# Kernel tuning notes

Hardware: AMD Instinct MI355X
Metric: run time of the kernel (lower is better)

## Reference

```python
import jax, jax.numpy as jnp
import numpy as np

N_NODES = 30000
N_EDGES = 480000
NEG_SLOPE = 0.2  # PyG GATConv default negative_slope


def setup_inputs() -> dict:
    key = jax.random.key(0)
    ks = jax.random.split(key, 10)

    def glorot(k, shape, fan):
        return jax.random.normal(k, shape, jnp.float32) * (1.0 / np.sqrt(fan))

    x = jax.random.normal(ks[0], (N_NODES, 1024), jnp.float32)
    edge_index = jax.random.randint(ks[1], (2, N_EDGES), 0, N_NODES)
    # layer 1: in=1024 -> heads=8, C=64, concat -> 512
    W1 = glorot(ks[2], (1024, 512), 1024)
    a1_src = glorot(ks[3], (8, 64), 64)
    a1_dst = glorot(ks[4], (8, 64), 64)
    b1 = jnp.zeros((512,), jnp.float32)
    # layer 2: in=512 -> heads=1, C=256, no concat
    W2 = glorot(ks[5], (512, 256), 512)
    a2_src = glorot(ks[6], (1, 256), 256)
    a2_dst = glorot(ks[7], (1, 256), 256)
    b2 = jnp.zeros((256,), jnp.float32)
    return {"x": x, "edge_index": edge_index, "W1": W1, "a1_src": a1_src,
            "a1_dst": a1_dst, "b1": b1, "W2": W2, "a2_src": a2_src,
            "a2_dst": a2_dst, "b2": b2}


def gat_conv(x, src, dst, W, a_src, a_dst, bias, heads, channels, concat):
    """PyG-style GATConv (self-loops already included in src/dst)."""
    n = x.shape[0]
    h = (x @ W).reshape(n, heads, channels)          # [N, H, C]
    al_s = jnp.einsum('nhc,hc->nh', h, a_src)        # per-node src logits
    al_d = jnp.einsum('nhc,hc->nh', h, a_dst)        # per-node dst logits
    e = jax.nn.leaky_relu(al_s[src] + al_d[dst], NEG_SLOPE)   # [E, H]
    # segment softmax over edges grouped by destination node
    m = jax.ops.segment_max(e, dst, num_segments=n)
    p = jnp.exp(e - m[dst])
    s = jax.ops.segment_sum(p, dst, num_segments=n)
    alpha = p / s[dst]                               # [E, H]
    out = jax.ops.segment_sum(alpha[:, :, None] * h[src], dst, num_segments=n)
    out = out.reshape(n, heads * channels) if concat else out.mean(axis=1)
    return out + bias


def reference(x, edge_index, W1, a1_src, a1_dst, b1, W2, a2_src, a2_dst, b2):
    n = x.shape[0]
    loops = jnp.arange(n, dtype=edge_index.dtype)
    src = jnp.concatenate([edge_index[0], loops])    # add self-loops (PyG default)
    dst = jnp.concatenate([edge_index[1], loops])
    # eval mode: dropout is identity
    h = jax.nn.elu(gat_conv(x, src, dst, W1, a1_src, a1_dst, b1, 8, 64, True))
    out = gat_conv(h, src, dst, W2, a2_src, a2_dst, b2, 1, 256, False)
    return out
```

## Files before the change

kernel.cpp:

```cpp
#include <hip/hip_runtime.h>
#include <hip/hip_bf16.h>

typedef unsigned int uint;
typedef unsigned short ushort;
typedef __attribute__((ext_vector_type(8))) short short8;
typedef __attribute__((ext_vector_type(4))) short short4v;
typedef __attribute__((ext_vector_type(4))) float f32x4;

#define LEAKY 0.2f

__device__ __forceinline__ ushort f2bf(float f) {
  __hip_bfloat16 h = __float2bfloat16(f);
  return __builtin_bit_cast(ushort, h);
}
__device__ __forceinline__ float bf2f(ushort u) {
  uint v = ((uint)u) << 16;
  return __builtin_bit_cast(float, v);
}
__device__ __forceinline__ void gload_lds16(const void* g, void* l) {
  __builtin_amdgcn_global_load_lds(
      (const __attribute__((address_space(1))) void*)g,
      (__attribute__((address_space(3))) void*)l, 16, 0, 0);
}

__global__ void convw(const float* __restrict__ W, ushort* __restrict__ Wt,
                      int K, int N) {
  int idx = blockIdx.x * 256 + threadIdx.x;
  if (idx >= K * N) return;
  int nrow = idx / K;
  int k = idx - nrow * K;
  Wt[idx] = f2bf(W[(size_t)k * N + nrow]);
}

__global__ void zero2(int* a, int* b, int n) {
  int i = blockIdx.x * 256 + threadIdx.x;
  if (i < n) { a[i] = 0; b[i] = 0; }
}

__global__ void hist(const int* __restrict__ dst, int E, int n, int* cnt) {
  int e = blockIdx.x * 256 + threadIdx.x;
  if (e >= E + n) return;
  int d = (e < E) ? dst[e] : (e - E);
  atomicAdd(&cnt[d], 1);
}

__global__ __launch_bounds__(1024) void scan_fast(const int* __restrict__ cnt,
                                                  int* __restrict__ rp, int n) {
  __shared__ int wsum[16];
  __shared__ int woff[16];
  const int t = threadIdx.x;
  const int per = (n + 1023) / 1024;
  const int base = t * per;
  int local[32];
  int s = 0;
#pragma unroll
  for (int i = 0; i < 32; i++) {
    if (i >= per) break;
    int idx = base + i;
    int v = (idx < n) ? cnt[idx] : 0;
    local[i] = s;
    s += v;
  }
  const int lane = t & 63, wave = t >> 6;
  int incl = s;
#pragma unroll
  for (int off = 1; off < 64; off <<= 1) {
    int v = __shfl_up(incl, off);
    if (lane >= off) incl += v;
  }
  if (lane == 63) wsum[wave] = incl;
  __syncthreads();
  if (wave == 0 && lane < 16) {
    int v = wsum[lane];
    int wi = v;
#pragma unroll
    for (int off = 1; off < 16; off <<= 1) {
      int u = __shfl_up(wi, off);
      if (lane >= off) wi += u;
    }
    woff[lane] = wi - v;
  }
  __syncthreads();
  const int gexcl = woff[wave] + (incl - s);
#pragma unroll
  for (int i = 0; i < 32; i++) {
    if (i >= per) break;
    int idx = base + i;
    if (idx < n) rp[idx] = gexcl + local[i];
  }
  if (t == 1023) rp[n] = woff[15] + incl;
}

__global__ void scatter(const int* __restrict__ src, const int* __restrict__ dst,
                        int E, int n, const int* __restrict__ rp,
                        int* fill, int* __restrict__ csr) {
  int e = blockIdx.x * 256 + threadIdx.x;
  if (e >= E + n) return;
  int s, d;
  if (e < E) { s = src[e]; d = dst[e]; } else { s = d = e - E; }
  int pos = rp[d] + atomicAdd(&fill[d], 1);
  csr[pos] = s;
}

template <int ABYTES>
__global__ __launch_bounds__(512) void gemm_wide(
    const void* __restrict__ Av, const ushort* __restrict__ Bt,
    ushort* __restrict__ C, int M, int K, int N) {
  constexpr int BM = 128, BN = 256, BK = 32;
  constexpr int SPRA = (BK * ABYTES) / 16;
  constexpr int A_ITER = (BM * SPRA) / 512;
  __shared__ __align__(16) char As[2][BM * BK * ABYTES];
  __shared__ __align__(16) char Bs[2][BN * BK * 2];
  const int tid = threadIdx.x;
  const int wave = tid >> 6, lane = tid & 63;
  const int g = lane >> 4, r16 = lane & 15;

  const int nwg = (int)gridDim.x;
  const int q = nwg >> 3, r = nwg & 7;
  const int xcd = (int)blockIdx.x & 7, pos = (int)blockIdx.x >> 3;
  const int wgid = (xcd < r ? xcd * (q + 1) : r * (q + 1) + (xcd - r) * q) + pos;

  const int nby = N / BN;
  const int bx = wgid / nby;
  const int by = wgid - bx * nby;
  const int bm = bx * BM, bn = by * BN;
  const int wm = (wave >> 2) * 64, wn = (wave & 3) * 64;

  f32x4 acc[4][4] = {};
  const char* A = (const char*)Av;

  auto stage = [&](int k0, int b) {
#pragma unroll
    for (int i = 0; i < A_ITER; i++) {
      int slot = i * 512 + tid;
      int row = slot / SPRA;
      int cp = slot % SPRA;
      int key = (ABYTES == 4) ? (row & 7) : ((row >> 1) & 3);
      int cl = cp ^ key;
      int arow = bm + row;
      arow = arow < M ? arow : M - 1;
      const char* gp = A + ((size_t)arow * K + k0) * ABYTES + cl * 16;
      char* lp = &As[b][0] + (i * 512 + wave * 64) * 16;
      gload_lds16(gp, lp);
    }
#pragma unroll
    for (int i = 0; i < 2; i++) {
      int slot = i * 512 + tid;
      int row = slot >> 2;
      int cp = slot & 3;
      int cl = cp ^ ((row >> 1) & 3);
      const char* gp = (const char*)(Bt + (size_t)(bn + row) * K + k0 + cl * 8);
      char* lp = &Bs[b][0] + (i * 512 + wave * 64) * 16;
      gload_lds16(gp, lp);
    }
  };

  const int nt = K / BK;
  stage(0, 0);
  int cur = 0;
  for (int t = 0; t < nt; ++t) {
    if (t + 1 < nt) {
      stage((t + 1) * BK, cur ^ 1);
      if constexpr (ABYTES == 4)
        asm volatile("s_waitcnt vmcnt(4)" ::: "memory");
      else
        asm volatile("s_waitcnt vmcnt(3)" ::: "memory");
    } else {
      asm volatile("s_waitcnt vmcnt(0)" ::: "memory");
    }
    __builtin_amdgcn_sched_barrier(0);
    __builtin_amdgcn_s_barrier();

    short8 af[4], bfr[4];
#pragma unroll
    for (int mi = 0; mi < 4; mi++) {
      int row = wm + mi * 16 + r16;
      if constexpr (ABYTES == 4) {
        int key = row & 7;
        f32x4 lo = *(const f32x4*)(&As[cur][0] + (row * 8 + ((2 * g) ^ key)) * 16);
        f32x4 hi = *(const f32x4*)(&As[cur][0] + (row * 8 + ((2 * g + 1) ^ key)) * 16);
        short8 s;
#pragma unroll
        for (int qq = 0; qq < 4; qq++) {
          s[qq] = (short)f2bf(lo[qq]);
          s[qq + 4] = (short)f2bf(hi[qq]);
        }
        af[mi] = s;
      } else {
        int key = (row >> 1) & 3;
        af[mi] = *(const short8*)(&As[cur][0] + (row * 4 + (g ^ key)) * 16);
      }
    }
#pragma unroll
    for (int ni = 0; ni < 4; ni++) {
      int row = wn + ni * 16 + r16;
      int key = (row >> 1) & 3;
      bfr[ni] = *(const short8*)(&Bs[cur][0] + (row * 4 + (g ^ key)) * 16);
    }
#pragma unroll
    for (int mi = 0; mi < 4; mi++)
#pragma unroll
      for (int ni = 0; ni < 4; ni++)
        acc[mi][ni] = __builtin_amdgcn_mfma_f32_16x16x32_bf16(
            af[mi], bfr[ni], acc[mi][ni], 0, 0, 0);
    __builtin_amdgcn_s_barrier();
    cur ^= 1;
  }

#pragma unroll
  for (int mi = 0; mi < 4; mi++) {
#pragma unroll
    for (int j = 0; j < 4; j++) {
      int row = bm + wm + mi * 16 + g * 4 + j;
      if (row < M) {
#pragma unroll
        for (int ni = 0; ni < 4; ni++) {
          int col = bn + wn + ni * 16 + r16;
          C[(size_t)row * N + col] = f2bf(acc[mi][ni][j]);
        }
      }
    }
  }
}

__global__ void logits1(const ushort* __restrict__ h1, const float* __restrict__ a_s,
                        const float* __restrict__ a_d, float* __restrict__ al_s,
                        float* __restrict__ al_d, int n) {
  int node = blockIdx.x * 4 + (threadIdx.x >> 6);
  if (node >= n) return;
  int lane = threadIdx.x & 63;
  int c0 = lane * 8;
  short8 hv = *(const short8*)&h1[(size_t)node * 512 + c0];
  float ps = 0.f, pd = 0.f;
#pragma unroll
  for (int j = 0; j < 8; j++) {
    float f = bf2f((ushort)hv[j]);
    ps += f * a_s[c0 + j];
    pd += f * a_d[c0 + j];
  }
#pragma unroll
  for (int m = 1; m < 8; m <<= 1) {
    ps += __shfl_xor(ps, m);
    pd += __shfl_xor(pd, m);
  }
  if ((lane & 7) == 0) {
    al_s[node * 8 + (lane >> 3)] = ps;
    al_d[node * 8 + (lane >> 3)] = pd;
  }
}

__global__ void logits2(const ushort* __restrict__ h2, const float* __restrict__ a_s,
                        const float* __restrict__ a_d, float* __restrict__ al_s,
                        float* __restrict__ al_d, int n) {
  int node = blockIdx.x * 4 + (threadIdx.x >> 6);
  if (node >= n) return;
  int lane = threadIdx.x & 63;
  int c0 = lane * 4;
  short4v hv = *(const short4v*)&h2[(size_t)node * 256 + c0];
  float ps = 0.f, pd = 0.f;
#pragma unroll
  for (int j = 0; j < 4; j++) {
    float f = bf2f((ushort)hv[j]);
    ps += f * a_s[c0 + j];
    pd += f * a_d[c0 + j];
  }
#pragma unroll
  for (int m = 1; m < 64; m <<= 1) {
    ps += __shfl_xor(ps, m);
    pd += __shfl_xor(pd, m);
  }
  if (lane == 0) {
    al_s[node] = ps;
    al_d[node] = pd;
  }
}

__global__ void agg1(const int* __restrict__ rp, const int* __restrict__ csr,
                     const ushort* __restrict__ h1, const float* __restrict__ al_s,
                     const float* __restrict__ al_d, const float* __restrict__ b1,
                     ushort* __restrict__ h2in, int n) {
  int node = blockIdx.x * 4 + (threadIdx.x >> 6);
  if (node >= n) return;
  int lane = threadIdx.x & 63;
  int head = lane >> 3, c0 = lane * 8;
  float ad = al_d[node * 8 + head];
  int beg = rp[node], end = rp[node + 1];
  float sum = 0.f;
  float acc[8] = {};
  int j = beg;
  for (; j + 4 <= end; j += 4) {
    int s0 = csr[j], s1 = csr[j + 1], s2 = csr[j + 2], s3 = csr[j + 3];
    float e0 = al_s[s0 * 8 + head] + ad;
    float e1 = al_s[s1 * 8 + head] + ad;
    float e2 = al_s[s2 * 8 + head] + ad;
    float e3 = al_s[s3 * 8 + head] + ad;
    short8 v0 = *(const short8*)&h1[(size_t)s0 * 512 + c0];
    short8 v1 = *(const short8*)&h1[(size_t)s1 * 512 + c0];
    short8 v2 = *(const short8*)&h1[(size_t)s2 * 512 + c0];
    short8 v3 = *(const short8*)&h1[(size_t)s3 * 512 + c0];
    e0 = e0 > 0.f ? e0 : LEAKY * e0;
    e1 = e1 > 0.f ? e1 : LEAKY * e1;
    e2 = e2 > 0.f ? e2 : LEAKY * e2;
    e3 = e3 > 0.f ? e3 : LEAKY * e3;
    float p0 = __expf(e0), p1 = __expf(e1), p2 = __expf(e2), p3 = __expf(e3);
    sum += (p0 + p1) + (p2 + p3);
#pragma unroll
    for (int qq = 0; qq < 8; qq++)
      acc[qq] += p0 * bf2f((ushort)v0[qq]) + p1 * bf2f((ushort)v1[qq]) +
                 p2 * bf2f((ushort)v2[qq]) + p3 * bf2f((ushort)v3[qq]);
  }
  for (; j < end; j++) {
    int s = csr[j];
    float e = al_s[s * 8 + head] + ad;
    e = e > 0.f ? e : LEAKY * e;
    float p = __expf(e);
    sum += p;
    short8 hv = *(const short8*)&h1[(size_t)s * 512 + c0];
#pragma unroll
    for (int qq = 0; qq < 8; qq++) acc[qq] += p * bf2f((ushort)hv[qq]);
  }
  float inv = 1.0f / sum;
  short8 o;
#pragma unroll
  for (int qq = 0; qq < 8; qq++) {
    float rr = acc[qq] * inv + b1[c0 + qq];
    rr = rr > 0.f ? rr : (__expf(rr) - 1.0f);
    o[qq] = (short)f2bf(rr);
  }
  *(short8*)&h2in[(size_t)node * 512 + c0] = o;
}

__global__ void agg2(const int* __restrict__ rp, const int* __restrict__ csr,
                     const ushort* __restrict__ h2, const float* __restrict__ al_s,
                     const float* __restrict__ al_d, const float* __restrict__ b2,
                     float* __restrict__ out, int n) {
  int node = blockIdx.x * 4 + (threadIdx.x >> 6);
  if (node >= n) return;
  int lane = threadIdx.x & 63;
  int c0 = lane * 4;
  float ad = al_d[node];
  int beg = rp[node], end = rp[node + 1];
  float sum = 0.f;
  float a0 = 0.f, a1 = 0.f, a2 = 0.f, a3 = 0.f;
  int j = beg;
  for (; j + 4 <= end; j += 4) {
    int s0 = csr[j], s1 = csr[j + 1], s2 = csr[j + 2], s3 = csr[j + 3];
    float e0 = al_s[s0] + ad;
    float e1 = al_s[s1] + ad;
    float e2 = al_s[s2] + ad;
    float e3 = al_s[s3] + ad;
    short4v v0 = *(const short4v*)&h2[(size_t)s0 * 256 + c0];
    short4v v1 = *(const short4v*)&h2[(size_t)s1 * 256 + c0];
    short4v v2 = *(const short4v*)&h2[(size_t)s2 * 256 + c0];
    short4v v3 = *(const short4v*)&h2[(size_t)s3 * 256 + c0];
    e0 = e0 > 0.f ? e0 : LEAKY * e0;
    e1 = e1 > 0.f ? e1 : LEAKY * e1;
    e2 = e2 > 0.f ? e2 : LEAKY * e2;
    e3 = e3 > 0.f ? e3 : LEAKY * e3;
    float p0 = __expf(e0), p1 = __expf(e1), p2 = __expf(e2), p3 = __expf(e3);
    sum += (p0 + p1) + (p2 + p3);
    a0 += p0 * bf2f((ushort)v0[0]) + p1 * bf2f((ushort)v1[0]) +
          p2 * bf2f((ushort)v2[0]) + p3 * bf2f((ushort)v3[0]);
    a1 += p0 * bf2f((ushort)v0[1]) + p1 * bf2f((ushort)v1[1]) +
          p2 * bf2f((ushort)v2[1]) + p3 * bf2f((ushort)v3[1]);
    a2 += p0 * bf2f((ushort)v0[2]) + p1 * bf2f((ushort)v1[2]) +
          p2 * bf2f((ushort)v2[2]) + p3 * bf2f((ushort)v3[2]);
    a3 += p0 * bf2f((ushort)v0[3]) + p1 * bf2f((ushort)v1[3]) +
          p2 * bf2f((ushort)v2[3]) + p3 * bf2f((ushort)v3[3]);
  }
  for (; j < end; j++) {
    int s = csr[j];
    float e = al_s[s] + ad;
    e = e > 0.f ? e : LEAKY * e;
    float p = __expf(e);
    sum += p;
    short4v hv = *(const short4v*)&h2[(size_t)s * 256 + c0];
    a0 += p * bf2f((ushort)hv[0]);
    a1 += p * bf2f((ushort)hv[1]);
    a2 += p * bf2f((ushort)hv[2]);
    a3 += p * bf2f((ushort)hv[3]);
  }
  float inv = 1.0f / sum;
  f32x4 o;
  o[0] = a0 * inv + b2[c0 + 0];
  o[1] = a1 * inv + b2[c0 + 1];
  o[2] = a2 * inv + b2[c0 + 2];
  o[3] = a3 * inv + b2[c0 + 3];
  *(f32x4*)&out[(size_t)node * 256 + c0] = o;
}

extern "C" void kernel_launch(void* const* d_in, const int* in_sizes, int n_in,
                              void* d_out, int out_size, void* d_ws, size_t ws_size,
                              hipStream_t stream) {
  const float* x = (const float*)d_in[0];
  const int* ei = (const int*)d_in[1];
  const float* W1 = (const float*)d_in[2];
  const float* a1s = (const float*)d_in[3];
  const float* a1d = (const float*)d_in[4];
  const float* b1 = (const float*)d_in[5];
  const float* W2 = (const float*)d_in[6];
  const float* a2s = (const float*)d_in[7];
  const float* a2d = (const float*)d_in[8];
  const float* b2 = (const float*)d_in[9];
  float* out = (float*)d_out;

  const int n = in_sizes[0] / 1024;
  const int E = in_sizes[1] / 2;
  const int K1 = 1024, C1 = 512, C2 = 256;

  char* ws = (char*)d_ws;
  ushort* h1 = (ushort*)(ws + 0);
  ushort* h2in = (ushort*)(ws + 31000000);
  ushort* h2 = (ushort*)(ws + 62000000);
  float* al_s = (float*)(ws + 78000000);
  float* al_d = (float*)(ws + 79000000);
  float* al2s = (float*)(ws + 80000000);
  float* al2d = (float*)(ws + 80200000);
  ushort* W1t = (ushort*)(ws + 80400000);
  ushort* W2t = (ushort*)(ws + 81600000);
  int* cnt = (int*)(ws + 82000000);
  int* rp = (int*)(ws + 82200000);
  int* fill = (int*)(ws + 82400000);
  int* csr = (int*)(ws + 82600000);

  const int* esrc = ei;
  const int* edst = ei + E;
  const int ET = E + n;

  convw<<<(C1 * K1 + 255) / 256, 256, 0, stream>>>(W1, W1t, K1, C1);
  convw<<<(C2 * C1 + 255) / 256, 256, 0, stream>>>(W2, W2t, C1, C2);
  zero2<<<(n + 255) / 256, 256, 0, stream>>>(cnt, fill, n);
  hist<<<(ET + 255) / 256, 256, 0, stream>>>(edst, E, n, cnt);
  scan_fast<<<1, 1024, 0, stream>>>(cnt, rp, n);
  scatter<<<(ET + 255) / 256, 256, 0, stream>>>(esrc, edst, E, n, rp, fill, csr);

  const int gx1 = ((n + 127) / 128) * (C1 / 256);
  gemm_wide<4><<<gx1, 512, 0, stream>>>(x, W1t, h1, n, K1, C1);
  logits1<<<(n + 3) / 4, 256, 0, stream>>>(h1, a1s, a1d, al_s, al_d, n);
  agg1<<<(n + 3) / 4, 256, 0, stream>>>(rp, csr, h1, al_s, al_d, b1, h2in, n);

  const int gx2 = ((n + 127) / 128) * (C2 / 256);
  gemm_wide<2><<<gx2, 512, 0, stream>>>(h2in, W2t, h2, n, C1, C2);
  logits2<<<(n + 3) / 4, 256, 0, stream>>>(h2, a2s, a2d, al2s, al2d, n);
  agg2<<<(n + 3) / 4, 256, 0, stream>>>(rp, csr, h2, al2s, al2d, b2, out, n);
}
```

Before: 282.3 us.

## Load GEMM B fragments directly from global memory and double BK

Stops staging the B (weight) tile in LDS; each wave now reads its B fragments straight from global memory into registers inside the k-loop. The K tile grows from 32 to 64, with two MFMA sub-steps per stage and a new swizzle for the wider A rows. This is meant to free LDS, halve the barrier/stage count and drop the B staging traffic. In exchange, the B global loads are not prefetched, so their latency is exposed, and waves sharing columns load the same B data redundantly.

```diff
diff --git a/kernel.cpp b/kernel.cpp
--- a/kernel.cpp
+++ b/kernel.cpp
@@ -106,11 +106,10 @@
 __global__ __launch_bounds__(512) void gemm_wide(
     const void* __restrict__ Av, const ushort* __restrict__ Bt,
     ushort* __restrict__ C, int M, int K, int N) {
-  constexpr int BM = 128, BN = 256, BK = 32;
+  constexpr int BM = 128, BN = 256, BK = 64;
   constexpr int SPRA = (BK * ABYTES) / 16;
   constexpr int A_ITER = (BM * SPRA) / 512;
   __shared__ __align__(16) char As[2][BM * BK * ABYTES];
-  __shared__ __align__(16) char Bs[2][BN * BK * 2];
   const int tid = threadIdx.x;
   const int wave = tid >> 6, lane = tid & 63;
   const int g = lane >> 4, r16 = lane & 15;
@@ -129,80 +128,82 @@
   f32x4 acc[4][4] = {};
   const char* A = (const char*)Av;
 
-  auto stage = [&](int k0, int b) {
+  auto stageA = [&](int k0, int b) {
 #pragma unroll
     for (int i = 0; i < A_ITER; i++) {
       int slot = i * 512 + tid;
       int row = slot / SPRA;
-      int cp = slot % SPRA;
-      int key = (ABYTES == 4) ? (row & 7) : ((row >> 1) & 3);
-      int cl = cp ^ key;
+      int cp = slot - row * SPRA;
+      int key = row & 7;
+      int cl;
+      if constexpr (ABYTES == 4)
+        cl = (cp & 8) | ((cp ^ key) & 7);
+      else
+        cl = cp ^ key;
       int arow = bm + row;
       arow = arow < M ? arow : M - 1;
       const char* gp = A + ((size_t)arow * K + k0) * ABYTES + cl * 16;
       char* lp = &As[b][0] + (i * 512 + wave * 64) * 16;
       gload_lds16(gp, lp);
     }
-#pragma unroll
-    for (int i = 0; i < 2; i++) {
-      int slot = i * 512 + tid;
-      int row = slot >> 2;
-      int cp = slot & 3;
-      int cl = cp ^ ((row >> 1) & 3);
-      const char* gp = (const char*)(Bt + (size_t)(bn + row) * K + k0 + cl * 8);
-      char* lp = &Bs[b][0] + (i * 512 + wave * 64) * 16;
-      gload_lds16(gp, lp);
-    }
   };
 
   const int nt = K / BK;
-  stage(0, 0);
+  stageA(0, 0);
   int cur = 0;
   for (int t = 0; t < nt; ++t) {
+    const int k0 = t * BK;
     if (t + 1 < nt) {
-      stage((t + 1) * BK, cur ^ 1);
+      stageA(k0 + BK, cur ^ 1);
       if constexpr (ABYTES == 4)
         asm volatile("s_waitcnt vmcnt(4)" ::: "memory");
       else
-        asm volatile("s_waitcnt vmcnt(3)" ::: "memory");
+        asm volatile("s_waitcnt vmcnt(2)" ::: "memory");
     } else {
       asm volatile("s_waitcnt vmcnt(0)" ::: "memory");
     }
     __builtin_amdgcn_sched_barrier(0);
     __builtin_amdgcn_s_barrier();
 
-    short8 af[4], bfr[4];
-#pragma unroll
-    for (int mi = 0; mi < 4; mi++) {
-      int row = wm + mi * 16 + r16;
-      if constexpr (ABYTES == 4) {
+#pragma unroll
+    for (int ksub = 0; ksub < 2; ksub++) {
+      short8 af[4];
+#pragma unroll
+      for (int mi = 0; mi < 4; mi++) {
+        int row = wm + mi * 16 + r16;
         int key = row & 7;
-        f32x4 lo = *(const f32x4*)(&As[cur][0] + (row * 8 + ((2 * g) ^ key)) * 16);
-        f32x4 hi = *(const f32x4*)(&As[cur][0] + (row * 8 + ((2 * g + 1) ^ key)) * 16);
-        short8 s;
-#pragma unroll
-        for (int qq = 0; qq < 4; qq++) {
-          s[qq] = (short)f2bf(lo[qq]);
-          s[qq + 4] = (short)f2bf(hi[qq]);
+        const char* base = &As[cur][0] + row * (SPRA * 16);
+        if constexpr (ABYTES == 4) {
+          int c0 = ksub * 8 + 2 * g;
+          int s0 = (c0 & 8) | ((c0 ^ key) & 7);
+          int s1 = ((c0 + 1) & 8) | (((c0 + 1) ^ key) & 7);
+          f32x4 lo = *(const f32x4*)(base + s0 * 16);
+          f32x4 hi = *(const f32x4*)(base + s1 * 16);
+          short8 s;
+#pragma unroll
+          for (int qq = 0; qq < 4; qq++) {
+            s[qq] = (short)f2bf(lo[qq]);
+            s[qq + 4] = (short)f2bf(hi[qq]);
+          }
+          af[mi] = s;
+        } else {
+          int c = ksub * 4 + g;
+          af[mi] = *(const short8*)(base + (c ^ key) * 16);
         }
-        af[mi] = s;
-      } else {
-        int key = (row >> 1) & 3;
-        af[mi] = *(const short8*)(&As[cur][0] + (row * 4 + (g ^ key)) * 16);
       }
+      short8 bfr[4];
+#pragma unroll
+      for (int ni = 0; ni < 4; ni++) {
+        int row = bn + wn + ni * 16 + r16;
+        bfr[ni] = *(const short8*)(Bt + (size_t)row * K + k0 + ksub * 32 + g * 8);
+      }
+#pragma unroll
+      for (int mi = 0; mi < 4; mi++)
+#pragma unroll
+        for (int ni = 0; ni < 4; ni++)
+          acc[mi][ni] = __builtin_amdgcn_mfma_f32_16x16x32_bf16(
+              af[mi], bfr[ni], acc[mi][ni], 0, 0, 0);
     }
-#pragma unroll
-    for (int ni = 0; ni < 4; ni++) {
-      int row = wn + ni * 16 + r16;
-      int key = (row >> 1) & 3;
-      bfr[ni] = *(const short8*)(&Bs[cur][0] + (row * 4 + (g ^ key)) * 16);
-    }
-#pragma unroll
-    for (int mi = 0; mi < 4; mi++)
-#pragma unroll
-      for (int ni = 0; ni < 4; ni++)
-        acc[mi][ni] = __builtin_amdgcn_mfma_f32_16x16x32_bf16(
-            af[mi], bfr[ni], acc[mi][ni], 0, 0, 0);
     __builtin_amdgcn_s_barrier();
     cur ^= 1;
   }
```

Result: slower. 326.1 us (+15.5%).

## Restructure GEMM: register-staged fp32 A conversion, BK=64, two waves per SIMD

Applied to the files above, without the earlier changes.

The GEMM kernel now loads the fp32 A tile into registers and converts it to bf16 once before writing it to LDS. Previously every wave converted fp32 to bf16 after reading from LDS, so the same elements were converted many times. BK doubles to 64 with a uniform XOR swizzle, which halves barrier count per K. It also adds launch_bounds occupancy 2, s_setprio around MFMAs, and drops the XCD-aware block remapping. The risks are register pressure from the occupancy hint, 64KB LDS (bf16 A 2x16KB plus B 2x32KB) fitting only two blocks, and the loss of L2 locality that the XCD remap gave.

```diff
diff --git a/kernel.cpp b/kernel.cpp
--- a/kernel.cpp
+++ b/kernel.cpp
@@ -103,107 +103,142 @@
 }
 
 template <int ABYTES>
-__global__ __launch_bounds__(512) void gemm_wide(
+__global__ __launch_bounds__(512, 2) void gemm_p2(
     const void* __restrict__ Av, const ushort* __restrict__ Bt,
     ushort* __restrict__ C, int M, int K, int N) {
-  constexpr int BM = 128, BN = 256, BK = 32;
-  constexpr int SPRA = (BK * ABYTES) / 16;
-  constexpr int A_ITER = (BM * SPRA) / 512;
-  __shared__ __align__(16) char As[2][BM * BK * ABYTES];
-  __shared__ __align__(16) char Bs[2][BN * BK * 2];
+  constexpr int BM = 128, BN = 256, BK = 64;
+  __shared__ __align__(16) ushort As[2][BM * BK];
+  __shared__ __align__(16) ushort Bs[2][BN * BK];
   const int tid = threadIdx.x;
   const int wave = tid >> 6, lane = tid & 63;
   const int g = lane >> 4, r16 = lane & 15;
-
-  const int nwg = (int)gridDim.x;
-  const int q = nwg >> 3, r = nwg & 7;
-  const int xcd = (int)blockIdx.x & 7, pos = (int)blockIdx.x >> 3;
-  const int wgid = (xcd < r ? xcd * (q + 1) : r * (q + 1) + (xcd - r) * q) + pos;
-
   const int nby = N / BN;
-  const int bx = wgid / nby;
-  const int by = wgid - bx * nby;
+  const int bx = (int)blockIdx.x / nby;
+  const int by = (int)blockIdx.x - bx * nby;
   const int bm = bx * BM, bn = by * BN;
   const int wm = (wave >> 2) * 64, wn = (wave & 3) * 64;
 
   f32x4 acc[4][4] = {};
-  const char* A = (const char*)Av;
-
-  auto stage = [&](int k0, int b) {
-#pragma unroll
-    for (int i = 0; i < A_ITER; i++) {
-      int slot = i * 512 + tid;
-      int row = slot / SPRA;
-      int cp = slot % SPRA;
-      int key = (ABYTES == 4) ? (row & 7) : ((row >> 1) & 3);
-      int cl = cp ^ key;
-      int arow = bm + row;
-      arow = arow < M ? arow : M - 1;
-      const char* gp = A + ((size_t)arow * K + k0) * ABYTES + cl * 16;
-      char* lp = &As[b][0] + (i * 512 + wave * 64) * 16;
-      gload_lds16(gp, lp);
-    }
+  const float* Af = (const float*)Av;
+  const ushort* Au = (const ushort*)Av;
+
+  const int arow_l = tid >> 2;
+  const int aq = tid & 3;
+  int arow_g = bm + arow_l;
+  arow_g = arow_g < M ? arow_g : M - 1;
+  f32x4 areg[4];
+
+  auto issueA4 = [&](int k0) {
+#pragma unroll
+    for (int i = 0; i < 4; i++)
+      areg[i] = *(const f32x4*)(Af + (size_t)arow_g * K + k0 + aq * 16 + i * 4);
+  };
+  auto writeA4 = [&](int b) {
+    short8 w0, w1;
+#pragma unroll
+    for (int j = 0; j < 4; j++) {
+      w0[j] = (short)f2bf(areg[0][j]);
+      w0[j + 4] = (short)f2bf(areg[1][j]);
+      w1[j] = (short)f2bf(areg[2][j]);
+      w1[j + 4] = (short)f2bf(areg[3][j]);
+    }
+    int key = arow_l & 7;
+    int s0 = (aq * 2) ^ key, s1 = (aq * 2 + 1) ^ key;
+    *(short8*)(&As[b][0] + (arow_l * 8 + s0) * 8) = w0;
+    *(short8*)(&As[b][0] + (arow_l * 8 + s1) * 8) = w1;
+  };
+  auto issueA2 = [&](int k0, int b) {
 #pragma unroll
     for (int i = 0; i < 2; i++) {
       int slot = i * 512 + tid;
-      int row = slot >> 2;
-      int cp = slot & 3;
-      int cl = cp ^ ((row >> 1) & 3);
-      const char* gp = (const char*)(Bt + (size_t)(bn + row) * K + k0 + cl * 8);
-      char* lp = &Bs[b][0] + (i * 512 + wave * 64) * 16;
-      gload_lds16(gp, lp);
+      int row = slot >> 3, cp = slot & 7;
+      int cl = cp ^ (row & 7);
+      int rg = bm + row;
+      rg = rg < M ? rg : M - 1;
+      const ushort* gp = Au + (size_t)rg * K + k0 + cl * 8;
+      gload_lds16(gp, &As[b][0] + (size_t)(i * 512 + wave * 64) * 8);
     }
   };
+  auto issueB = [&](int k0, int b) {
+#pragma unroll
+    for (int i = 0; i < 4; i++) {
+      int slot = i * 512 + tid;
+      int row = slot >> 3, cp = slot & 7;
+      int cl = cp ^ (row & 7);
+      const ushort* gp = Bt + (size_t)(bn + row) * K + k0 + cl * 8;
+      gload_lds16(gp, &Bs[b][0] + (size_t)(i * 512 + wave * 64) * 8);
+    }
+  };
 
   const int nt = K / BK;
-  stage(0, 0);
+  if constexpr (ABYTES == 4) {
+    issueA4(0);
+    __builtin_amdgcn_sched_barrier(0);
+    issueB(0, 0);
+    __builtin_amdgcn_sched_barrier(0);
+    asm volatile("s_waitcnt vmcnt(4)" ::: "memory");
+    __builtin_amdgcn_sched_barrier(0);
+    writeA4(0);
+  } else {
+    issueA2(0, 0);
+    issueB(0, 0);
+  }
+
   int cur = 0;
   for (int t = 0; t < nt; ++t) {
+    const int k0 = t * BK;
     if (t + 1 < nt) {
-      stage((t + 1) * BK, cur ^ 1);
-      if constexpr (ABYTES == 4)
-        asm volatile("s_waitcnt vmcnt(4)" ::: "memory");
-      else
-        asm volatile("s_waitcnt vmcnt(3)" ::: "memory");
+      if constexpr (ABYTES == 4) {
+        issueA4(k0 + BK);
+        __builtin_amdgcn_sched_barrier(0);
+        issueB(k0 + BK, cur ^ 1);
+        __builtin_amdgcn_sched_barrier(0);
+        asm volatile("s_waitcnt vmcnt(8)" ::: "memory");
+      } else {
+        issueA2(k0 + BK, cur ^ 1);
+        issueB(k0 + BK, cur ^ 1);
+        asm volatile("s_waitcnt vmcnt(6)" ::: "memory");
+      }
     } else {
       asm volatile("s_waitcnt vmcnt(0)" ::: "memory");
     }
+    asm volatile("s_waitcnt lgkmcnt(0)" ::: "memory");
     __builtin_amdgcn_sched_barrier(0);
     __builtin_amdgcn_s_barrier();
 
-    short8 af[4], bfr[4];
-#pragma unroll
-    for (int mi = 0; mi < 4; mi++) {
-      int row = wm + mi * 16 + r16;
-      if constexpr (ABYTES == 4) {
-        int key = row & 7;
-        f32x4 lo = *(const f32x4*)(&As[cur][0] + (row * 8 + ((2 * g) ^ key)) * 16);
-        f32x4 hi = *(const f32x4*)(&As[cur][0] + (row * 8 + ((2 * g + 1) ^ key)) * 16);
-        short8 s;
-#pragma unroll
-        for (int qq = 0; qq < 4; qq++) {
-          s[qq] = (short)f2bf(lo[qq]);
-          s[qq + 4] = (short)f2bf(hi[qq]);
-        }
-        af[mi] = s;
-      } else {
-        int key = (row >> 1) & 3;
-        af[mi] = *(const short8*)(&As[cur][0] + (row * 4 + (g ^ key)) * 16);
+#pragma unroll
+    for (int ks = 0; ks < 2; ks++) {
+      short8 af[4], bfr[4];
+#pragma unroll
+      for (int mi = 0; mi < 4; mi++) {
+        int row = wm + mi * 16 + r16;
+        int slot = (ks * 4 + g) ^ (row & 7);
+        af[mi] = *(const short8*)(&As[cur][0] + (row * 8 + slot) * 8);
       }
-    }
-#pragma unroll
-    for (int ni = 0; ni < 4; ni++) {
-      int row = wn + ni * 16 + r16;
-      int key = (row >> 1) & 3;
-      bfr[ni] = *(const short8*)(&Bs[cur][0] + (row * 4 + (g ^ key)) * 16);
-    }
-#pragma unroll
-    for (int mi = 0; mi < 4; mi++)
-#pragma unroll
-      for (int ni = 0; ni < 4; ni++)
-        acc[mi][ni] = __builtin_amdgcn_mfma_f32_16x16x32_bf16(
-            af[mi], bfr[ni], acc[mi][ni], 0, 0, 0);
+#pragma unroll
+      for (int ni = 0; ni < 4; ni++) {
+        int row = wn + ni * 16 + r16;
+        int slot = (ks * 4 + g) ^ (row & 7);
+        bfr[ni] = *(const short8*)(&Bs[cur][0] + (row * 8 + slot) * 8);
+      }
+      __builtin_amdgcn_s_setprio(1);
+#pragma unroll
+      for (int mi = 0; mi < 4; mi++)
+#pragma unroll
+        for (int ni = 0; ni < 4; ni++)
+          acc[mi][ni] = __builtin_amdgcn_mfma_f32_16x16x32_bf16(
+              af[mi], bfr[ni], acc[mi][ni], 0, 0, 0);
+      __builtin_amdgcn_s_setprio(0);
+    }
     __builtin_amdgcn_s_barrier();
+
+    if constexpr (ABYTES == 4) {
+      if (t + 1 < nt) {
+        asm volatile("s_waitcnt vmcnt(4)" ::: "memory");
+        __builtin_amdgcn_sched_barrier(0);
+        writeA4(cur ^ 1);
+      }
+    }
     cur ^= 1;
   }
 
@@ -435,12 +470,12 @@
   scatter<<<(ET + 255) / 256, 256, 0, stream>>>(esrc, edst, E, n, rp, fill, csr);
 
   const int gx1 = ((n + 127) / 128) * (C1 / 256);
-  gemm_wide<4><<<gx1, 512, 0, stream>>>(x, W1t, h1, n, K1, C1);
+  gemm_p2<4><<<gx1, 512, 0, stream>>>(x, W1t, h1, n, K1, C1);
   logits1<<<(n + 3) / 4, 256, 0, stream>>>(h1, a1s, a1d, al_s, al_d, n);
   agg1<<<(n + 3) / 4, 256, 0, stream>>>(rp, csr, h1, al_s, al_d, b1, h2in, n);
 
   const int gx2 = ((n + 127) / 128) * (C2 / 256);
-  gemm_wide<2><<<gx2, 512, 0, stream>>>(h2in, W2t, h2, n, C1, C2);
+  gemm_p2<2><<<gx2, 512, 0, stream>>>(h2in, W2t, h2, n, C1, C2);
   logits2<<<(n + 3) / 4, 256, 0, stream>>>(h2, a2s, a2d, al2s, al2d, n);
   agg2<<<(n + 3) / 4, 256, 0, stream>>>(rp, csr, h2, al2s, al2d, b2, out, n);
 }
```

Result: slower. 292.3 us (+3.6%).
